# Optimization experiments

Measured on AMD Instinct MI355X. Metric: run time of the kernel, lower is better.

## Reference

```python
import jax, jax.numpy as jnp
import numpy as np

B, S, D, H = 4, 2048, 2048, 16
HD = D // H  # 128


def _rope(t, cos, sin):
    # t: [B, S, H, HD]; cos/sin: [S, HD//2]
    tr = t.reshape(t.shape[:-1] + (HD // 2, 2))
    t1, t2 = tr[..., 0], tr[..., 1]
    c = cos[None, :, None, :]
    s = sin[None, :, None, :]
    o1 = t1 * c - t2 * s
    o2 = t1 * s + t2 * c
    return jnp.stack([o1, o2], axis=-1).reshape(t.shape)


def setup_inputs() -> dict:
    key = jax.random.key(0)
    ks = jax.random.split(key, 9)
    init_std = HD ** -0.5
    pos = jnp.arange(S, dtype=jnp.float32)[:, None]
    inv = 1.0 / (10000.0 ** (jnp.arange(0, HD, 2, dtype=jnp.float32) / HD))
    ang = pos * inv[None, :]
    return {
        "x": jax.random.normal(ks[0], (B, S, D), jnp.float32),
        "query": jax.random.normal(ks[1], (B, S, D), jnp.float32),
        "value": jax.random.normal(ks[2], (B, S, D), jnp.float32),
        "freqs_cos": jnp.cos(ang),
        "freqs_sin": jnp.sin(ang),
        "key_w": jax.random.normal(ks[3], (D, D), jnp.float32) * init_std,
        "key_b": jnp.zeros((D,), jnp.float32),
        "proj_w": jax.random.normal(ks[4], (D, D), jnp.float32) * init_std,
        "proj_b": jnp.zeros((D,), jnp.float32),
    }


def reference(x, query, value, freqs_cos, freqs_sin, key_w, key_b, proj_w, proj_b):
    # key projection applied to x; query/value arrive pre-projected
    k = (jnp.einsum("bsd,ed->bse", x, key_w) + key_b).reshape(B, S, H, HD)
    q = query.reshape(B, S, H, HD)
    v = value.reshape(B, S, H, HD)
    q = _rope(q, freqs_cos, freqs_sin)
    k = _rope(k, freqs_cos, freqs_sin)
    scale = 1.0 / np.sqrt(HD)
    scores = jnp.einsum("bqhd,bkhd->bhqk", q, k) * scale  # [B,H,S,S]
    causal = jnp.tril(jnp.ones((S, S), bool))
    scores = jnp.where(causal[None, None], scores, jnp.finfo(scores.dtype).min)
    probs = jax.nn.softmax(scores, axis=-1)
    out = jnp.einsum("bhqk,bkhd->bqhd", probs, v).reshape(B, S, D)
    return jnp.einsum("bsd,ed->bse", out, proj_w) + proj_b
```

## Files before the change

kernel.cpp:

```cpp
#include <hip/hip_runtime.h>
#include <hip/hip_bf16.h>
#include <stdint.h>

#define BB 4
#define SS 2048
#define DD 2048
#define HH 16
#define HD 128
#define MTOT (BB*SS)

typedef __attribute__((ext_vector_type(8))) short short8;
typedef __attribute__((ext_vector_type(4))) float f32x4;

__device__ __forceinline__ unsigned short f2bf(float f) {
    union { float f; unsigned int u; } v; v.f = f;
    unsigned int u = v.u;
    return (unsigned short)((u + 0x7FFFu + ((u >> 16) & 1u)) >> 16);
}
__device__ __forceinline__ unsigned short f2bf_ru(float f) {
    union { float f; unsigned int u; } v; v.f = f;
    return (unsigned short)((v.u + 0x8000u) >> 16);
}

__global__ __launch_bounds__(256) void convert_kernel(
    const float* __restrict__ src, unsigned short* __restrict__ dst, int n4) {
    int i = blockIdx.x * 256 + threadIdx.x;
    if (i >= n4) return;
    float4 v = ((const float4*)src)[i];
    unsigned int lo = (unsigned int)f2bf(v.x) | ((unsigned int)f2bf(v.y) << 16);
    unsigned int hi = (unsigned int)f2bf(v.z) | ((unsigned int)f2bf(v.w) << 16);
    ((uint2*)dst)[i] = make_uint2(lo, hi);
}

__global__ __launch_bounds__(256) void rope_q_kernel(
    const float* __restrict__ q, const float* __restrict__ fc,
    const float* __restrict__ fs, unsigned short* __restrict__ dst) {
    const float scl2 = 0.08838834764831845f * 1.44269504088896f;
    int idx = blockIdx.x * 256 + threadIdx.x;
    int row   = idx >> 10;
    int s     = row & (SS - 1);
    int p     = idx & 63;
    float2 t = ((const float2*)q)[idx];
    float c = fc[s*64 + p], sn = fs[s*64 + p];
    float o1 = (t.x*c - t.y*sn) * scl2;
    float o2 = (t.x*sn + t.y*c) * scl2;
    ((unsigned int*)dst)[idx] = (unsigned int)f2bf(o1) | ((unsigned int)f2bf(o2) << 16);
}

__global__ __launch_bounds__(256) void transpose_v_kernel(
    const float* __restrict__ v, unsigned short* __restrict__ vt) {
    __shared__ unsigned short tile[64][72];
    int bh = blockIdx.z;
    int s0 = blockIdx.x * 64, d0 = blockIdx.y * 64;
    int t = threadIdx.x;
    #pragma unroll
    for (int it = 0; it < 4; ++it) {
        int i  = it*16 + (t >> 4);
        int j4 = t & 15;
        float4 f = *(const float4*)(v +
            (((size_t)((bh >> 4)*SS + s0 + i)*HH + (bh & 15))*HD + d0 + j4*4));
        unsigned int lo = (unsigned int)f2bf(f.x) | ((unsigned int)f2bf(f.y) << 16);
        unsigned int hi = (unsigned int)f2bf(f.z) | ((unsigned int)f2bf(f.w) << 16);
        *(uint2*)&tile[i][j4*4] = make_uint2(lo, hi);
    }
    __syncthreads();
    unsigned int* vt32 = (unsigned int*)vt;
    #pragma unroll
    for (int it = 0; it < 8; ++it) {
        int task = it*256 + t;
        int tt = task & 31;
        int d  = task >> 5;
        int slo = ((tt & 1) << 5) + (tt >> 1);
        unsigned int lo = tile[slo][d], hi = tile[slo + 16][d];
        vt32[((size_t)bh*HD + d0 + d)*(SS/2) + (s0 >> 1) + tt] = lo | (hi << 16);
    }
}

template<int MODE>
__global__ __launch_bounds__(256, 3) void gemm_kernel(
    const unsigned short* __restrict__ A, const unsigned short* __restrict__ W,
    const float* __restrict__ bias, const float* __restrict__ fc,
    const float* __restrict__ fs, void* __restrict__ out)
{
    __shared__ unsigned short As[128*64];
    __shared__ unsigned short Bs[128*64];
    const int K = DD;
    int L   = blockIdx.y * 16 + blockIdx.x;
    int swz = (L & 7) * 128 + (L >> 3);
    int m0 = (swz >> 4) * 128, n0 = (swz & 15) * 128;
    int t = threadIdx.x, lane = t & 63, w = t >> 6;
    int wm = w >> 1, wn = w & 1;
    int l15 = lane & 15, quad = lane >> 4;
    int l7 = l15 & 7;

    f32x4 acc[4][4] = {};

    for (int k0 = 0; k0 < K; k0 += 64) {
        __syncthreads();
        #pragma unroll
        for (int i = 0; i < 4; ++i) {
            int ci  = i*256 + t;
            int row = ci >> 3;
            int cc  = ci & 7;
            int gch = cc ^ (row & 7);
            const unsigned short* ga = A + (size_t)(m0 + row) * K + k0 + gch*8;
            const unsigned short* gb = W + (size_t)(n0 + row) * K + k0 + gch*8;
            unsigned short* la = As + (size_t)(i*256 + w*64) * 8;
            unsigned short* lb = Bs + (size_t)(i*256 + w*64) * 8;
            __builtin_amdgcn_global_load_lds(
                (__attribute__((address_space(1))) void*)(uintptr_t)ga,
                (__attribute__((address_space(3))) void*)la, 16, 0, 0);
            __builtin_amdgcn_global_load_lds(
                (__attribute__((address_space(1))) void*)(uintptr_t)gb,
                (__attribute__((address_space(3))) void*)lb, 16, 0, 0);
        }
        __syncthreads();

        #pragma unroll
        for (int kk = 0; kk < 2; ++kk) {
            short8 af[4], bw[4];
            #pragma unroll
            for (int i = 0; i < 4; ++i) {
                int ch = (kk*4 + quad) ^ l7;
                af[i] = *(const short8*)(As + (size_t)(wm*64 + i*16 + l15)*64 + ch*8);
                bw[i] = *(const short8*)(Bs + (size_t)(wn*64 + i*16 + l15)*64 + ch*8);
            }
            #pragma unroll
            for (int i = 0; i < 4; ++i)
                #pragma unroll
                for (int j = 0; j < 4; ++j)
                    acc[i][j] = __builtin_amdgcn_mfma_f32_16x16x32_bf16(
                        af[i], bw[j], acc[i][j], 0, 0, 0);
        }
    }

    #pragma unroll
    for (int i = 0; i < 4; ++i) {
        #pragma unroll
        for (int j = 0; j < 4; ++j) {
            int col = n0 + wn*64 + j*16 + l15;
            float bv = bias[col];
            #pragma unroll
            for (int r = 0; r < 4; ++r) {
                int row = m0 + wm*64 + i*16 + quad*4 + r;
                float v = acc[i][j][r] + bv;
                if (MODE == 0) {
                    int s = row & (SS - 1);
                    int p = (col & 127) >> 1;
                    float other = __shfl_xor(v, 1);
                    float c = fc[s*64 + p], sn = fs[s*64 + p];
                    float res = (col & 1) ? (other*sn + v*c) : (v*c - other*sn);
                    ((unsigned short*)out)[(size_t)row*DD + col] = f2bf(res);
                } else {
                    ((float*)out)[(size_t)row*DD + col] = v;
                }
            }
        }
    }
}

__global__ __launch_bounds__(512, 4) void attn_kernel(
    const unsigned short* __restrict__ Q, const unsigned short* __restrict__ Kr,
    const unsigned short* __restrict__ Vt, unsigned short* __restrict__ O)
{
    constexpr int PSTR = 72;
    __shared__ unsigned short Ks[2*64*128];
    __shared__ unsigned short VTs[128*64];
    __shared__ unsigned short Ps[128*PSTR];

    int L   = blockIdx.y * 8 + blockIdx.x;
    int swz = (L & 7) * 64 + (L >> 3);
    int bh   = swz >> 3;
    int pair = swz & 7;

    int b = bh >> 4, h = bh & 15;
    size_t base  = (size_t)b*SS*DD + (size_t)h*HD;
    size_t vbase = (size_t)bh*HD*SS;

    int t = threadIdx.x, lane = t & 63, w = t >> 6;
    int l15 = lane & 15, quad = lane >> 4;
    int l7 = l15 & 7;

    auto stageK = [&](int jt, int buf) {
        int j0s = jt * 64;
        #pragma unroll
        for (int i = 0; i < 2; ++i) {
            int ci  = i*512 + t;
            int row = ci >> 4;
            int cc  = ci & 15;
            int gch = cc ^ (row & 7);
            const unsigned short* ga = Kr + base + (size_t)(j0s + row)*DD + gch*8;
            unsigned short* la = Ks + buf*(64*128) + (size_t)(i*512 + w*64)*8;
            __builtin_amdgcn_global_load_lds(
                (__attribute__((address_space(1))) void*)(uintptr_t)ga,
                (__attribute__((address_space(3))) void*)la, 16, 0, 0);
        }
    };
    auto stageV = [&](int jt) {
        int j0s = jt * 64;
        #pragma unroll
        for (int i = 0; i < 2; ++i) {
            int ci  = i*512 + t;
            int d   = ci >> 3;
            int cc  = ci & 7;
            int gch = cc ^ (d & 7);
            const unsigned short* ga = Vt + vbase + (size_t)d*SS + j0s + gch*8;
            unsigned short* la = VTs + (size_t)(i*512 + w*64)*8;
            __builtin_amdgcn_global_load_lds(
                (__attribute__((address_space(1))) void*)(uintptr_t)ga,
                (__attribute__((address_space(3))) void*)la, 16, 0, 0);
        }
    };

    for (int ph = 0; ph < 2; ++ph) {
        int qt = ph ? (15 - pair) : pair;
        int q0 = qt * 128;
        int rw = q0 + w*16;

        short8 aq[4];
        #pragma unroll
        for (int kk = 0; kk < 4; ++kk)
            aq[kk] = *(const short8*)(Q + base +
                (size_t)(rw + l15)*DD + kk*32 + quad*8);

        float m_i[4], l_lane[4];
        #pragma unroll
        for (int r = 0; r < 4; ++r) { m_i[r] = -1e30f; l_lane[r] = 0.f; }
        f32x4 o_acc[8] = {};

        __syncthreads();
        stageK(0, 0);
        int jmax = 2*qt + 1;

        for (int jt = 0; jt <= jmax; ++jt) {
            int pb = jt & 1;
            int j0 = jt * 64;
            const unsigned short* Kb = Ks + pb*(64*128);

            __syncthreads();
            stageV(jt);
            __builtin_amdgcn_sched_barrier(0);
            if (jt < jmax) stageK(jt + 1, pb ^ 1);

            bool active = (j0 <= rw + 15);
            if (active) {
                f32x4 sacc[4];
                #pragma unroll
                for (int c = 0; c < 4; ++c) {
                    sacc[c] = (f32x4){0.f, 0.f, 0.f, 0.f};
                    #pragma unroll
                    for (int kk = 0; kk < 4; ++kk) {
                        short8 bk = *(const short8*)(Kb +
                            (size_t)(c*16 + l15)*128 + ((kk*4 + quad) ^ l7)*8);
                        sacc[c] = __builtin_amdgcn_mfma_f32_16x16x32_bf16(aq[kk], bk, sacc[c], 0,0,0);
                    }
                }

                bool diag = (j0 + 63 > rw);
                float pp[4][4], mt4[4];
                #pragma unroll
                for (int c = 0; c < 4; ++c)
                    #pragma unroll
                    for (int r = 0; r < 4; ++r) {
                        float v = sacc[c][r];
                        if (diag) {
                            int cg = j0 + c*16 + l15;
                            int rg = rw + quad*4 + r;
                            if (cg > rg) v = -1e30f;
                        }
                        pp[c][r] = v;
                    }
                #pragma unroll
                for (int r = 0; r < 4; ++r)
                    mt4[r] = fmaxf(fmaxf(pp[0][r], pp[1][r]), fmaxf(pp[2][r], pp[3][r]));

                bool growl = false;
                #pragma unroll
                for (int r = 0; r < 4; ++r)
                    growl = growl || (mt4[r] > m_i[r] + 8.0f);
                if (__any(growl)) {
                    #pragma unroll
                    for (int r = 0; r < 4; ++r) {
                        float m = mt4[r];
                        m = fmaxf(m, __shfl_xor(m, 1));
                        m = fmaxf(m, __shfl_xor(m, 2));
                        m = fmaxf(m, __shfl_xor(m, 4));
                        m = fmaxf(m, __shfl_xor(m, 8));
                        float mn = fmaxf(m_i[r], m);
                        float a  = exp2f(m_i[r] - mn);
                        m_i[r] = mn;
                        l_lane[r] *= a;
                        mt4[r] = a;
                    }
                    #pragma unroll
                    for (int f = 0; f < 8; ++f)
                        #pragma unroll
                        for (int r = 0; r < 4; ++r)
                            o_acc[f][r] *= mt4[r];
                }

                #pragma unroll
                for (int r = 0; r < 4; ++r) {
                    float e0 = exp2f(pp[0][r] - m_i[r]);
                    float e1 = exp2f(pp[1][r] - m_i[r]);
                    float e2 = exp2f(pp[2][r] - m_i[r]);
                    float e3 = exp2f(pp[3][r] - m_i[r]);
                    l_lane[r] += (e0 + e1) + (e2 + e3);
                    unsigned int lo = (unsigned int)f2bf_ru(e0) | ((unsigned int)f2bf_ru(e1) << 16);
                    unsigned int hi = (unsigned int)f2bf_ru(e2) | ((unsigned int)f2bf_ru(e3) << 16);
                    *(uint2*)&Ps[(size_t)(w*16 + quad*4 + r)*PSTR + l15*4] = make_uint2(lo, hi);
                }
            }

            __builtin_amdgcn_sched_barrier(0);
            if (jt < jmax) { asm volatile("s_waitcnt vmcnt(2)" ::: "memory"); }
            else           { asm volatile("s_waitcnt vmcnt(0)" ::: "memory"); }
            __builtin_amdgcn_s_barrier();
            __builtin_amdgcn_sched_barrier(0);

            if (active) {
                #pragma unroll
                for (int kk2 = 0; kk2 < 2; ++kk2) {
                    short8 ap = *(const short8*)(Ps + (size_t)(w*16 + l15)*PSTR + kk2*32 + quad*8);
                    #pragma unroll
                    for (int f = 0; f < 8; ++f) {
                        short8 bv = *(const short8*)(VTs +
                            (size_t)(f*16 + l15)*64 + ((kk2*4 + quad) ^ l7)*8);
                        o_acc[f] = __builtin_amdgcn_mfma_f32_16x16x32_bf16(ap, bv, o_acc[f], 0,0,0);
                    }
                }
            }
        }

        #pragma unroll
        for (int r = 0; r < 4; ++r) {
            float s = l_lane[r];
            s += __shfl_xor(s, 1);
            s += __shfl_xor(s, 2);
            s += __shfl_xor(s, 4);
            s += __shfl_xor(s, 8);
            float inv = 1.0f / s;
            int srow = rw + quad*4 + r;
            #pragma unroll
            for (int f = 0; f < 8; ++f) {
                int d = f*16 + l15;
                O[base + (size_t)srow*DD + d] = f2bf(o_acc[f][r] * inv);
            }
        }
    }
}

extern "C" void kernel_launch(void* const* d_in, const int* in_sizes, int n_in,
                              void* d_out, int out_size, void* d_ws, size_t ws_size,
                              hipStream_t stream) {
    const float* x      = (const float*)d_in[0];
    const float* query  = (const float*)d_in[1];
    const float* value  = (const float*)d_in[2];
    const float* fc     = (const float*)d_in[3];
    const float* fs     = (const float*)d_in[4];
    const float* key_w  = (const float*)d_in[5];
    const float* key_b  = (const float*)d_in[6];
    const float* proj_w = (const float*)d_in[7];
    const float* proj_b = (const float*)d_in[8];

    const int ND  = BB*SS*DD;
    const int NW  = DD*DD;
    unsigned short* xb  = (unsigned short*)d_ws;
    unsigned short* kwb = xb  + ND;
    unsigned short* pwb = kwb + NW;
    unsigned short* qr  = pwb + NW;
    unsigned short* vt  = qr  + ND;
    unsigned short* kr  = vt  + ND;
    unsigned short* ao  = xb;

    convert_kernel<<<ND/4/256, 256, 0, stream>>>(x, xb, ND/4);
    convert_kernel<<<NW/4/256, 256, 0, stream>>>(key_w, kwb, NW/4);
    convert_kernel<<<NW/4/256, 256, 0, stream>>>(proj_w, pwb, NW/4);
    rope_q_kernel<<<ND/2/256, 256, 0, stream>>>(query, fc, fs, qr);
    transpose_v_kernel<<<dim3(SS/64, HD/64, BB*HH), 256, 0, stream>>>(value, vt);

    dim3 gg(DD/128, MTOT/128);
    gemm_kernel<0><<<gg, 256, 0, stream>>>(xb, kwb, key_b, fc, fs, (void*)kr);
    attn_kernel<<<dim3(8, BB*HH), 512, 0, stream>>>(qr, kr, vt, ao);
    gemm_kernel<1><<<gg, 256, 0, stream>>>(ao, pwb, proj_b, nullptr, nullptr, d_out);
}
```

Baseline: 544.4 us.

## Double-buffer GEMM LDS tiles and use hardware bf16 pack in attention

Measured after the change: 561.4 us. 3.1% more time.

```diff
diff --git a/kernel.cpp b/kernel.cpp
--- a/kernel.cpp
+++ b/kernel.cpp
@@ -16,10 +16,6 @@
     union { float f; unsigned int u; } v; v.f = f;
     unsigned int u = v.u;
     return (unsigned short)((u + 0x7FFFu + ((u >> 16) & 1u)) >> 16);
-}
-__device__ __forceinline__ unsigned short f2bf_ru(float f) {
-    union { float f; unsigned int u; } v; v.f = f;
-    return (unsigned short)((v.u + 0x8000u) >> 16);
 }
 
 __global__ __launch_bounds__(256) void convert_kernel(
@@ -77,13 +73,13 @@
 }
 
 template<int MODE>
-__global__ __launch_bounds__(256, 3) void gemm_kernel(
+__global__ __launch_bounds__(256, 2) void gemm_kernel(
     const unsigned short* __restrict__ A, const unsigned short* __restrict__ W,
     const float* __restrict__ bias, const float* __restrict__ fc,
     const float* __restrict__ fs, void* __restrict__ out)
 {
-    __shared__ unsigned short As[128*64];
-    __shared__ unsigned short Bs[128*64];
+    __shared__ unsigned short As[2*128*64];
+    __shared__ unsigned short Bs[2*128*64];
     const int K = DD;
     int L   = blockIdx.y * 16 + blockIdx.x;
     int swz = (L & 7) * 128 + (L >> 3);
@@ -95,18 +91,17 @@
 
     f32x4 acc[4][4] = {};
 
-    for (int k0 = 0; k0 < K; k0 += 64) {
-        __syncthreads();
+    auto stage = [&](int k0s, int buf) {
         #pragma unroll
         for (int i = 0; i < 4; ++i) {
             int ci  = i*256 + t;
             int row = ci >> 3;
             int cc  = ci & 7;
             int gch = cc ^ (row & 7);
-            const unsigned short* ga = A + (size_t)(m0 + row) * K + k0 + gch*8;
-            const unsigned short* gb = W + (size_t)(n0 + row) * K + k0 + gch*8;
-            unsigned short* la = As + (size_t)(i*256 + w*64) * 8;
-            unsigned short* lb = Bs + (size_t)(i*256 + w*64) * 8;
+            const unsigned short* ga = A + (size_t)(m0 + row) * K + k0s + gch*8;
+            const unsigned short* gb = W + (size_t)(n0 + row) * K + k0s + gch*8;
+            unsigned short* la = As + buf*(128*64) + (size_t)(i*256 + w*64) * 8;
+            unsigned short* lb = Bs + buf*(128*64) + (size_t)(i*256 + w*64) * 8;
             __builtin_amdgcn_global_load_lds(
                 (__attribute__((address_space(1))) void*)(uintptr_t)ga,
                 (__attribute__((address_space(3))) void*)la, 16, 0, 0);
@@ -114,16 +109,24 @@
                 (__attribute__((address_space(1))) void*)(uintptr_t)gb,
                 (__attribute__((address_space(3))) void*)lb, 16, 0, 0);
         }
+    };
+
+    stage(0, 0);
+    for (int k0 = 0; k0 < K; k0 += 64) {
+        int pb = (k0 >> 6) & 1;
         __syncthreads();
-
+        if (k0 + 64 < K) stage(k0 + 64, pb ^ 1);
+
+        const unsigned short* Ab = As + pb*(128*64);
+        const unsigned short* Bb = Bs + pb*(128*64);
         #pragma unroll
         for (int kk = 0; kk < 2; ++kk) {
             short8 af[4], bw[4];
             #pragma unroll
             for (int i = 0; i < 4; ++i) {
                 int ch = (kk*4 + quad) ^ l7;
-                af[i] = *(const short8*)(As + (size_t)(wm*64 + i*16 + l15)*64 + ch*8);
-                bw[i] = *(const short8*)(Bs + (size_t)(wn*64 + i*16 + l15)*64 + ch*8);
+                af[i] = *(const short8*)(Ab + (size_t)(wm*64 + i*16 + l15)*64 + ch*8);
+                bw[i] = *(const short8*)(Bb + (size_t)(wn*64 + i*16 + l15)*64 + ch*8);
             }
             #pragma unroll
             for (int i = 0; i < 4; ++i)
@@ -306,8 +309,9 @@
                     float e2 = exp2f(pp[2][r] - m_i[r]);
                     float e3 = exp2f(pp[3][r] - m_i[r]);
                     l_lane[r] += (e0 + e1) + (e2 + e3);
-                    unsigned int lo = (unsigned int)f2bf_ru(e0) | ((unsigned int)f2bf_ru(e1) << 16);
-                    unsigned int hi = (unsigned int)f2bf_ru(e2) | ((unsigned int)f2bf_ru(e3) << 16);
+                    unsigned int lo, hi;
+                    asm("v_cvt_pk_bf16_f32 %0, %1, %2" : "=v"(lo) : "v"(e0), "v"(e1));
+                    asm("v_cvt_pk_bf16_f32 %0, %1, %2" : "=v"(hi) : "v"(e2), "v"(e3));
                     *(uint2*)&Ps[(size_t)(w*16 + quad*4 + r)*PSTR + l15*4] = make_uint2(lo, hi);
                 }
             }
```

## Enlarge GEMM tiles to 256x256 with 512 threads and double-buffered LDS

Applied to the files above, without the earlier changes.

After: 545.7 us. Within noise of the previous version (+0.2%).

```diff
diff --git a/kernel.cpp b/kernel.cpp
--- a/kernel.cpp
+++ b/kernel.cpp
@@ -77,36 +77,36 @@
 }
 
 template<int MODE>
-__global__ __launch_bounds__(256, 3) void gemm_kernel(
+__global__ __launch_bounds__(512, 2) void gemm_kernel(
     const unsigned short* __restrict__ A, const unsigned short* __restrict__ W,
     const float* __restrict__ bias, const float* __restrict__ fc,
     const float* __restrict__ fs, void* __restrict__ out)
 {
-    __shared__ unsigned short As[128*64];
-    __shared__ unsigned short Bs[128*64];
+    __shared__ unsigned short As[2*256*64];
+    __shared__ unsigned short Bs[2*256*64];
     const int K = DD;
-    int L   = blockIdx.y * 16 + blockIdx.x;
-    int swz = (L & 7) * 128 + (L >> 3);
-    int m0 = (swz >> 4) * 128, n0 = (swz & 15) * 128;
+    int L   = blockIdx.y * 8 + blockIdx.x;
+    int swz = (L & 7) * 32 + (L >> 3);
+    int m0 = (swz >> 3) * 256, n0 = (swz & 7) * 256;
     int t = threadIdx.x, lane = t & 63, w = t >> 6;
-    int wm = w >> 1, wn = w & 1;
+    int wm = w >> 2, wn = w & 3;
     int l15 = lane & 15, quad = lane >> 4;
     int l7 = l15 & 7;
 
-    f32x4 acc[4][4] = {};
-
-    for (int k0 = 0; k0 < K; k0 += 64) {
-        __syncthreads();
-        #pragma unroll
-        for (int i = 0; i < 4; ++i) {
-            int ci  = i*256 + t;
+    f32x4 acc[8][4] = {};
+
+    auto stage = [&](int kt, int buf) {
+        int kb = kt * 64;
+        #pragma unroll
+        for (int jj = 0; jj < 4; ++jj) {
+            int ci  = jj*512 + t;
             int row = ci >> 3;
             int cc  = ci & 7;
             int gch = cc ^ (row & 7);
-            const unsigned short* ga = A + (size_t)(m0 + row) * K + k0 + gch*8;
-            const unsigned short* gb = W + (size_t)(n0 + row) * K + k0 + gch*8;
-            unsigned short* la = As + (size_t)(i*256 + w*64) * 8;
-            unsigned short* lb = Bs + (size_t)(i*256 + w*64) * 8;
+            const unsigned short* ga = A + (size_t)(m0 + row) * K + kb + gch*8;
+            const unsigned short* gb = W + (size_t)(n0 + row) * K + kb + gch*8;
+            unsigned short* la = As + buf*(256*64) + (size_t)(jj*512 + w*64) * 8;
+            unsigned short* lb = Bs + buf*(256*64) + (size_t)(jj*512 + w*64) * 8;
             __builtin_amdgcn_global_load_lds(
                 (__attribute__((address_space(1))) void*)(uintptr_t)ga,
                 (__attribute__((address_space(3))) void*)la, 16, 0, 0);
@@ -114,35 +114,48 @@
                 (__attribute__((address_space(1))) void*)(uintptr_t)gb,
                 (__attribute__((address_space(3))) void*)lb, 16, 0, 0);
         }
+    };
+
+    stage(0, 0);
+    __syncthreads();
+    const int NT = K / 64;
+    for (int kt = 0; kt < NT; ++kt) {
+        int pb = kt & 1;
+        if (kt + 1 < NT) stage(kt + 1, pb ^ 1);
+        __builtin_amdgcn_sched_barrier(0);
+
+        const unsigned short* Ab = As + pb*(256*64);
+        const unsigned short* Bb = Bs + pb*(256*64);
+        short8 bw[4][2];
+        #pragma unroll
+        for (int j = 0; j < 4; ++j)
+            #pragma unroll
+            for (int kk = 0; kk < 2; ++kk)
+                bw[j][kk] = *(const short8*)(Bb +
+                    (size_t)(wn*64 + j*16 + l15)*64 + (((kk*4 + quad) ^ l7)*8));
+        #pragma unroll
+        for (int i = 0; i < 8; ++i) {
+            const unsigned short* ar = Ab + (size_t)(wm*128 + i*16 + l15)*64;
+            short8 a0 = *(const short8*)(ar + ((quad     ^ l7)*8));
+            short8 a1 = *(const short8*)(ar + (((4+quad) ^ l7)*8));
+            #pragma unroll
+            for (int j = 0; j < 4; ++j) {
+                acc[i][j] = __builtin_amdgcn_mfma_f32_16x16x32_bf16(a0, bw[j][0], acc[i][j], 0,0,0);
+                acc[i][j] = __builtin_amdgcn_mfma_f32_16x16x32_bf16(a1, bw[j][1], acc[i][j], 0,0,0);
+            }
+        }
         __syncthreads();
-
-        #pragma unroll
-        for (int kk = 0; kk < 2; ++kk) {
-            short8 af[4], bw[4];
-            #pragma unroll
-            for (int i = 0; i < 4; ++i) {
-                int ch = (kk*4 + quad) ^ l7;
-                af[i] = *(const short8*)(As + (size_t)(wm*64 + i*16 + l15)*64 + ch*8);
-                bw[i] = *(const short8*)(Bs + (size_t)(wn*64 + i*16 + l15)*64 + ch*8);
-            }
-            #pragma unroll
-            for (int i = 0; i < 4; ++i)
-                #pragma unroll
-                for (int j = 0; j < 4; ++j)
-                    acc[i][j] = __builtin_amdgcn_mfma_f32_16x16x32_bf16(
-                        af[i], bw[j], acc[i][j], 0, 0, 0);
-        }
     }
 
     #pragma unroll
-    for (int i = 0; i < 4; ++i) {
+    for (int i = 0; i < 8; ++i) {
         #pragma unroll
         for (int j = 0; j < 4; ++j) {
             int col = n0 + wn*64 + j*16 + l15;
             float bv = bias[col];
             #pragma unroll
             for (int r = 0; r < 4; ++r) {
-                int row = m0 + wm*64 + i*16 + quad*4 + r;
+                int row = m0 + wm*128 + i*16 + quad*4 + r;
                 float v = acc[i][j][r] + bv;
                 if (MODE == 0) {
                     int s = row & (SS - 1);
@@ -379,8 +392,8 @@
     rope_q_kernel<<<ND/2/256, 256, 0, stream>>>(query, fc, fs, qr);
     transpose_v_kernel<<<dim3(SS/64, HD/64, BB*HH), 256, 0, stream>>>(value, vt);
 
-    dim3 gg(DD/128, MTOT/128);
-    gemm_kernel<0><<<gg, 256, 0, stream>>>(xb, kwb, key_b, fc, fs, (void*)kr);
+    dim3 gg(DD/256, MTOT/256);
+    gemm_kernel<0><<<gg, 512, 0, stream>>>(xb, kwb, key_b, fc, fs, (void*)kr);
     attn_kernel<<<dim3(8, BB*HH), 512, 0, stream>>>(qr, kr, vt, ao);
-    gemm_kernel<1><<<gg, 256, 0, stream>>>(ao, pwb, proj_b, nullptr, nullptr, d_out);
-}
+    gemm_kernel<1><<<gg, 512, 0, stream>>>(ao, pwb, proj_b, nullptr, nullptr, d_out);
+}
```
